# Kernel tuning notes

Hardware: AMD Instinct MI355X
Metric: run time of the kernel (lower is better)

Reference implementation:

```python
import jax, jax.numpy as jnp
import numpy as np

N_NODES = 100000
N_EDGES = 1600000
IN_CH = 64
HID = 64
N_GRAPHS = 64


def _sage_conv(x, src, dst, Wl, bl, Wr, n_nodes):
    # PyG SAGEConv (aggr='mean'): out = lin_l(mean_{j in N(i)} x_j) + lin_r(x_i)
    msg = x[src]                                            # [E, d] gather
    agg = jax.ops.segment_sum(msg, dst, num_segments=n_nodes)
    cnt = jax.ops.segment_sum(jnp.ones((src.shape[0],), x.dtype), dst,
                              num_segments=n_nodes)
    agg = agg / jnp.maximum(cnt, 1.0)[:, None]
    return agg @ Wl + bl + x @ Wr


def setup_inputs() -> dict:
    key = jax.random.key(0)
    ks = jax.random.split(key, 16)
    x = jax.random.normal(ks[0], (N_NODES, IN_CH), jnp.float32)
    edge_index = jax.random.randint(ks[1], (2, N_EDGES), 0, N_NODES, jnp.int64)
    batch = jnp.sort(jax.random.randint(ks[2], (N_NODES,), 0, N_GRAPHS, jnp.int64))

    def glorot(k, fan_in, fan_out):
        s = jnp.sqrt(2.0 / (fan_in + fan_out))
        return jax.random.normal(k, (fan_in, fan_out), jnp.float32) * s

    params = {
        'W1l': glorot(ks[3], IN_CH, HID), 'b1': jnp.zeros((HID,), jnp.float32),
        'W1r': glorot(ks[4], IN_CH, HID),
        'W2l': glorot(ks[5], HID, HID), 'b2': jnp.zeros((HID,), jnp.float32),
        'W2r': glorot(ks[6], HID, HID),
        'W3l': glorot(ks[7], HID, HID), 'b3': jnp.zeros((HID,), jnp.float32),
        'W3r': glorot(ks[8], HID, HID),
        'Wc1': glorot(ks[9], HID, HID // 2), 'bc1': jnp.zeros((HID // 2,), jnp.float32),
        'Wc2': glorot(ks[10], HID // 2, 2), 'bc2': jnp.zeros((2,), jnp.float32),
    }
    return {'x': x, 'edge_index': edge_index, 'batch': batch, **params}


def reference(x, edge_index, batch,
              W1l, b1, W1r, W2l, b2, W2r, W3l, b3, W3r,
              Wc1, bc1, Wc2, bc2):
    src, dst = edge_index[0], edge_index[1]
    n = x.shape[0]
    h = jax.nn.relu(_sage_conv(x, src, dst, W1l, b1, W1r, n))   # dropout = identity (eval)
    h = jax.nn.relu(_sage_conv(h, src, dst, W2l, b2, W2r, n))
    h = jax.nn.relu(_sage_conv(h, src, dst, W3l, b3, W3r, n))
    # global mean pool over graphs
    sums = jax.ops.segment_sum(h, batch, num_segments=N_GRAPHS)
    cnts = jax.ops.segment_sum(jnp.ones((n,), h.dtype), batch, num_segments=N_GRAPHS)
    g = sums / jnp.maximum(cnts, 1.0)[:, None]                  # [G, HID]
    # MLP head (dropout = identity at eval)
    return jax.nn.relu(g @ Wc1 + bc1) @ Wc2 + bc2               # [G, 2]
```

## Files before the change

kernel.cpp:

```cpp
#include <hip/hip_runtime.h>
#include <hip/hip_bf16.h>
#include <hip/hip_fp16.h>

typedef unsigned int u32;
typedef unsigned short u16;
typedef _Float16 f16x8 __attribute__((ext_vector_type(8)));
typedef float f32x4 __attribute__((ext_vector_type(4)));

#define NBLK1 512
#define MMBLK 256

__device__ __forceinline__ u16 f2h(float f) { return __half_as_ushort(__float2half(f)); }
__device__ __forceinline__ u32 packh2(float a, float b) {
    return (u32)f2h(a) | ((u32)f2h(b) << 16);
}
__device__ __forceinline__ __half2 sx(__half2 v, int m) {
    int iv = __shfl_xor(*(int*)&v, m, 64);
    return *(__half2*)&iv;
}

__device__ __forceinline__ int gidx(const void* p, long long i, int w64) {
    if (w64) return (int)((const long long*)p)[i];
    return ((const int*)p)[i];
}

__device__ __forceinline__ int detect_w64(const int* edge_words, int E, int tid, int* sh) {
    if (tid == 0) *sh = 0;
    __syncthreads();
    const long long totalWords = 2LL * E;
    const long long step = totalWords / 256;
    long long w = ((long long)tid * step) | 1;
    int nz = (w < totalWords) ? edge_words[w] : 0;
    if (nz) atomicOr(sh, 1);
    __syncthreads();
    return (*sh) ? 0 : 1;
}

__global__ void __launch_bounds__(256) fused_hist_mm1(
        const void* __restrict__ edge, int* __restrict__ flag, u32* __restrict__ ticket,
        u32* __restrict__ HG, int E, int n, int nb1,
        const float* __restrict__ X, const float* __restrict__ Wl,
        const float* __restrict__ Wr, const float* __restrict__ Bv,
        u16* __restrict__ Z, u16* __restrict__ R) {
    if (blockIdx.x < NBLK1) {
        __shared__ u32 h[256];
        __shared__ int shnz;
        const int tid = threadIdx.x;
        h[tid] = 0;
        const int w64 = detect_w64((const int*)edge, E, tid, &shnz);
        if (blockIdx.x == 0 && tid == 0) { flag[0] = w64; ticket[0] = 0; }
        __syncthreads();
        const int chunk = (E + NBLK1 - 1) / NBLK1;
        const int s = blockIdx.x * chunk;
        const int e = min(s + chunk, E);
        for (int i = s + tid; i < e; i += 256) {
            int d = gidx(edge, (long long)E + i, w64);
            if ((unsigned)d >= (unsigned)n) d = 0;
            atomicAdd(&h[d >> 9], 1);
        }
        __syncthreads();
        for (int b = tid; b < nb1; b += 256) HG[b * NBLK1 + blockIdx.x] = h[b];
        return;
    }
    const int lane = threadIdx.x & 63;
    const int quad = lane >> 4;
    const int m16 = lane & 15;
    f16x8 bl[2][4], br[2][4];
#pragma unroll
    for (int kh = 0; kh < 2; ++kh)
#pragma unroll
        for (int t = 0; t < 4; ++t)
#pragma unroll
            for (int j = 0; j < 8; ++j) {
                int k = kh * 32 + quad * 8 + j;
                int c = t * 16 + m16;
                bl[kh][t][j] = (_Float16)Wl[k * 64 + c];
                br[kh][t][j] = (_Float16)Wr[k * 64 + c];
            }
    float bias_t[4];
#pragma unroll
    for (int t = 0; t < 4; ++t) bias_t[t] = Bv[t * 16 + m16];

    const int ntiles = (n + 15) >> 4;
    const int nwaves = (gridDim.x - NBLK1) * 4;
    for (int tile = (blockIdx.x - NBLK1) * 4 + (threadIdx.x >> 6); tile < ntiles; tile += nwaves) {
        const int nodeBase = tile << 4;
        int nodeA = nodeBase + m16;
        if (nodeA >= n) nodeA = n - 1;
        f16x8 a[2];
#pragma unroll
        for (int kh = 0; kh < 2; ++kh) {
            const float4* p = (const float4*)(X + (size_t)nodeA * 64 + kh * 32 + quad * 8);
            float4 x0 = p[0], x1 = p[1];
            a[kh][0] = (_Float16)x0.x; a[kh][1] = (_Float16)x0.y;
            a[kh][2] = (_Float16)x0.z; a[kh][3] = (_Float16)x0.w;
            a[kh][4] = (_Float16)x1.x; a[kh][5] = (_Float16)x1.y;
            a[kh][6] = (_Float16)x1.z; a[kh][7] = (_Float16)x1.w;
        }
        f32x4 cl[4], cr[4];
#pragma unroll
        for (int t = 0; t < 4; ++t) {
            f32x4 c0 = {0.f, 0.f, 0.f, 0.f};
            c0 = __builtin_amdgcn_mfma_f32_16x16x32_f16(a[0], bl[0][t], c0, 0, 0, 0);
            c0 = __builtin_amdgcn_mfma_f32_16x16x32_f16(a[1], bl[1][t], c0, 0, 0, 0);
            cl[t] = c0;
            f32x4 c1 = {0.f, 0.f, 0.f, 0.f};
            c1 = __builtin_amdgcn_mfma_f32_16x16x32_f16(a[0], br[0][t], c1, 0, 0, 0);
            c1 = __builtin_amdgcn_mfma_f32_16x16x32_f16(a[1], br[1][t], c1, 0, 0, 0);
            cr[t] = c1;
        }
#pragma unroll
        for (int rg = 0; rg < 4; ++rg) {
            const int node = nodeBase + quad * 4 + rg;
            if (node < n) {
#pragma unroll
                for (int t = 0; t < 4; ++t) {
                    const int c = t * 16 + m16;
                    Z[(size_t)node * 64 + c] = f2h(cl[t][rg]);
                    R[(size_t)node * 64 + c] = f2h(cr[t][rg] + bias_t[t]);
                }
            }
        }
    }
}

__global__ void scanAB(u32* __restrict__ HG, u32* __restrict__ blockSums,
                       u32* __restrict__ SB, u32* __restrict__ ticket, int n) {
    __shared__ u32 ts[256];
    __shared__ int isLast;
    const int ITEMS = 8;
    const int tid = threadIdx.x;
    int base = blockIdx.x * 2048 + tid * ITEMS;
    u32 v[ITEMS];
    u32 sum = 0;
#pragma unroll
    for (int i = 0; i < ITEMS; ++i) {
        int idx = base + i;
        v[i] = (idx < n) ? HG[idx] : 0;
        sum += v[i];
    }
    ts[tid] = sum;
    __syncthreads();
    u32 incl = sum;
    for (int d = 1; d < 256; d <<= 1) {
        u32 y = 0;
        if (tid >= d) y = ts[tid - d];
        __syncthreads();
        incl += y;
        ts[tid] = incl;
        __syncthreads();
    }
    u32 run = incl - sum;
#pragma unroll
    for (int i = 0; i < ITEMS; ++i) {
        int idx = base + i;
        if (idx < n) HG[idx] = run;
        run += v[i];
    }
    if (tid == 255) {
        atomicExch(&blockSums[blockIdx.x], incl);
        __threadfence();
        u32 t = atomicAdd(&ticket[0], 1u);
        isLast = (t == gridDim.x - 1);
    }
    __syncthreads();
    if (!isLast) return;
    const int nb = gridDim.x;
    u32 bv = (tid < nb) ? atomicAdd(&blockSums[tid], 0u) : 0;
    ts[tid] = bv;
    __syncthreads();
    u32 bincl = bv;
    for (int d = 1; d < 256; d <<= 1) {
        u32 y = 0;
        if (tid >= d) y = ts[tid - d];
        __syncthreads();
        bincl += y;
        ts[tid] = bincl;
        __syncthreads();
    }
    if (tid < nb) SB[tid] = bincl - bv;
}

__global__ void __launch_bounds__(256) p1_scatter(const void* __restrict__ edge,
                                                  const int* __restrict__ flag,
                                                  const u32* __restrict__ HG,
                                                  const u32* __restrict__ SB,
                                                  u32* __restrict__ P, int E, int n, int nb1) {
    __shared__ u32 base[256];
    __shared__ u32 cur[256];
    const int tid = threadIdx.x;
    cur[tid] = 0;
    for (int b = tid; b < nb1; b += 256) {
        int i = b * NBLK1 + blockIdx.x;
        base[b] = HG[i] + SB[i >> 11];
    }
    __syncthreads();
    const int w64 = flag[0];
    const int chunk = (E + NBLK1 - 1) / NBLK1;
    const int s = blockIdx.x * chunk;
    const int e = min(s + chunk, E);
    for (int i = s + tid; i < e; i += 256) {
        int d = gidx(edge, (long long)E + i, w64);
        if ((unsigned)d >= (unsigned)n) d = 0;
        int sv = gidx(edge, i, w64);
        if ((unsigned)sv >= (unsigned)n) sv = 0;
        const int b1 = d >> 9;
        u32 r = atomicAdd(&cur[b1], 1);
        P[base[b1] + r] = (u32)sv | ((u32)(d & 511) << 17);
    }
}

__global__ void __launch_bounds__(256) p2_kernel(const u32* __restrict__ P,
                                                 const u32* __restrict__ HG,
                                                 const u32* __restrict__ SB,
                                                 u32* __restrict__ offs,
                                                 int* __restrict__ ss,
                                                 float* __restrict__ pool,
                                                 int E, int n, int nb1) {
    __shared__ u32 h2[512];
    __shared__ u32 ts[256];
    const int tid = threadIdx.x;
    const int b = blockIdx.x;
    if (b == 0)
        for (int i = tid; i < 4096; i += 256) pool[i] = 0.f;
    const int i0 = b * NBLK1;
    const int bs = (int)(HG[i0] + SB[i0 >> 11]);
    int be;
    if (b + 1 < nb1) {
        const int i1 = (b + 1) * NBLK1;
        be = (int)(HG[i1] + SB[i1 >> 11]);
    } else be = E;
    h2[tid] = 0;
    h2[tid + 256] = 0;
    __syncthreads();
    for (int i = bs + tid; i < be; i += 256) atomicAdd(&h2[(P[i] >> 17) & 511], 1);
    __syncthreads();
    u32 v0 = h2[2 * tid], v1 = h2[2 * tid + 1];
    u32 sum = v0 + v1;
    ts[tid] = sum;
    __syncthreads();
    u32 incl = sum;
    for (int d = 1; d < 256; d <<= 1) {
        u32 y = 0;
        if (tid >= d) y = ts[tid - d];
        __syncthreads();
        incl += y;
        ts[tid] = incl;
        __syncthreads();
    }
    u32 run = incl - sum;
    h2[2 * tid] = run;
    h2[2 * tid + 1] = run + v0;
    const int node0 = b * 512 + 2 * tid;
    if (node0 < n) offs[node0] = bs + run;
    if (node0 + 1 < n) offs[node0 + 1] = bs + run + v0;
    if (b == 0 && tid == 0) offs[n] = (u32)E;
    __syncthreads();
    for (int i = bs + tid; i < be; i += 256) {
        u32 p = P[i];
        u32 r = atomicAdd(&h2[(p >> 17) & 511], 1);
        ss[bs + r] = (int)(p & 0x1FFFFu);
    }
}

__global__ void __launch_bounds__(256) mm_mfma_kernel(const u16* __restrict__ X,
                                                      const float* __restrict__ Wl,
                                                      const float* __restrict__ Wr,
                                                      const float* __restrict__ Bv,
                                                      u16* __restrict__ Z,
                                                      u16* __restrict__ R, int n) {
    const int lane = threadIdx.x & 63;
    const int quad = lane >> 4;
    const int m16 = lane & 15;
    f16x8 bl[2][4], br[2][4];
#pragma unroll
    for (int kh = 0; kh < 2; ++kh)
#pragma unroll
        for (int t = 0; t < 4; ++t)
#pragma unroll
            for (int j = 0; j < 8; ++j) {
                int k = kh * 32 + quad * 8 + j;
                int c = t * 16 + m16;
                bl[kh][t][j] = (_Float16)Wl[k * 64 + c];
                br[kh][t][j] = (_Float16)Wr[k * 64 + c];
            }
    float bias_t[4];
#pragma unroll
    for (int t = 0; t < 4; ++t) bias_t[t] = Bv[t * 16 + m16];

    const int ntiles = (n + 15) >> 4;
    const int nwaves = gridDim.x * 4;
    for (int tile = blockIdx.x * 4 + (threadIdx.x >> 6); tile < ntiles; tile += nwaves) {
        const int nodeBase = tile << 4;
        int nodeA = nodeBase + m16;
        if (nodeA >= n) nodeA = n - 1;
        const _Float16* xp = (const _Float16*)X + (size_t)nodeA * 64;
        f16x8 a[2];
#pragma unroll
        for (int kh = 0; kh < 2; ++kh)
            a[kh] = *(const f16x8*)(xp + kh * 32 + quad * 8);
        f32x4 cl[4], cr[4];
#pragma unroll
        for (int t = 0; t < 4; ++t) {
            f32x4 c0 = {0.f, 0.f, 0.f, 0.f};
            c0 = __builtin_amdgcn_mfma_f32_16x16x32_f16(a[0], bl[0][t], c0, 0, 0, 0);
            c0 = __builtin_amdgcn_mfma_f32_16x16x32_f16(a[1], bl[1][t], c0, 0, 0, 0);
            cl[t] = c0;
            f32x4 c1 = {0.f, 0.f, 0.f, 0.f};
            c1 = __builtin_amdgcn_mfma_f32_16x16x32_f16(a[0], br[0][t], c1, 0, 0, 0);
            c1 = __builtin_amdgcn_mfma_f32_16x16x32_f16(a[1], br[1][t], c1, 0, 0, 0);
            cr[t] = c1;
        }
#pragma unroll
        for (int rg = 0; rg < 4; ++rg) {
            const int node = nodeBase + quad * 4 + rg;
            if (node < n) {
#pragma unroll
                for (int t = 0; t < 4; ++t) {
                    const int c = t * 16 + m16;
                    Z[(size_t)node * 64 + c] = f2h(cl[t][rg]);
                    R[(size_t)node * 64 + c] = f2h(cr[t][rg] + bias_t[t]);
                }
            }
        }
    }
}

__global__ void __launch_bounds__(256) agg_kernel(const u16* __restrict__ Zin,
                                                  const u16* __restrict__ Rin,
                                                  const u32* __restrict__ offs,
                                                  const int* __restrict__ ss,
                                                  u16* __restrict__ Hout, int n) {
    const int lane = threadIdx.x & 63;
    const int oct = lane >> 3;
    const int sub = lane & 7;
    const uint4* Z16 = (const uint4*)Zin;
    const int node = (blockIdx.x << 2) | (threadIdx.x >> 6);
    if (node >= n) return;
    const int off = (int)offs[node], end = (int)offs[node + 1];
    const int deg = end - off;
    const __half2 zero2 = __float2half2_rn(0.f);
    const __half2 one2 = __float2half2_rn(1.f);
    __half2 a0 = zero2, a1 = zero2, a2 = zero2, a3 = zero2;
    __half2 b0 = zero2, b1 = zero2, b2 = zero2, b3 = zero2;
    for (int base = off; base < end; base += 64) {
        const int cnt = min(64, end - base);
        const int idx = ss[base + (lane < cnt ? lane : cnt - 1)];
        int p = 0;
        for (; p + 16 <= cnt; p += 16) {
            int s0 = __shfl(idx, p + oct, 64);
            int s1 = __shfl(idx, p + 8 + oct, 64);
            uint4 u0 = Z16[(size_t)s0 * 8 + sub];
            uint4 u1 = Z16[(size_t)s1 * 8 + sub];
            a0 = __hadd2(a0, *(const __half2*)&u0.x);
            a1 = __hadd2(a1, *(const __half2*)&u0.y);
            a2 = __hadd2(a2, *(const __half2*)&u0.z);
            a3 = __hadd2(a3, *(const __half2*)&u0.w);
            b0 = __hadd2(b0, *(const __half2*)&u1.x);
            b1 = __hadd2(b1, *(const __half2*)&u1.y);
            b2 = __hadd2(b2, *(const __half2*)&u1.z);
            b3 = __hadd2(b3, *(const __half2*)&u1.w);
        }
        const int rem = cnt - p;
        if (rem) {
            int j = p + oct;
            int s0 = __shfl(idx, j < cnt ? j : cnt - 1, 64);
            uint4 u0 = Z16[(size_t)s0 * 8 + sub];
            __half2 m0 = (j < cnt) ? one2 : zero2;
            a0 = __hfma2(*(const __half2*)&u0.x, m0, a0);
            a1 = __hfma2(*(const __half2*)&u0.y, m0, a1);
            a2 = __hfma2(*(const __half2*)&u0.z, m0, a2);
            a3 = __hfma2(*(const __half2*)&u0.w, m0, a3);
            if (rem > 8) {
                int j1 = p + 8 + oct;
                int s1 = __shfl(idx, j1 < cnt ? j1 : cnt - 1, 64);
                uint4 u1 = Z16[(size_t)s1 * 8 + sub];
                __half2 m1 = (j1 < cnt) ? one2 : zero2;
                b0 = __hfma2(*(const __half2*)&u1.x, m1, b0);
                b1 = __hfma2(*(const __half2*)&u1.y, m1, b1);
                b2 = __hfma2(*(const __half2*)&u1.z, m1, b2);
                b3 = __hfma2(*(const __half2*)&u1.w, m1, b3);
            }
        }
    }
    a0 = __hadd2(a0, b0); a1 = __hadd2(a1, b1);
    a2 = __hadd2(a2, b2); a3 = __hadd2(a3, b3);
    a0 = __hadd2(a0, sx(a0, 8));  a1 = __hadd2(a1, sx(a1, 8));
    a2 = __hadd2(a2, sx(a2, 8));  a3 = __hadd2(a3, sx(a3, 8));
    a0 = __hadd2(a0, sx(a0, 16)); a1 = __hadd2(a1, sx(a1, 16));
    a2 = __hadd2(a2, sx(a2, 16)); a3 = __hadd2(a3, sx(a3, 16));
    a0 = __hadd2(a0, sx(a0, 32)); a1 = __hadd2(a1, sx(a1, 32));
    a2 = __hadd2(a2, sx(a2, 32)); a3 = __hadd2(a3, sx(a3, 32));
    if (oct == 0) {
        const uint4* R16 = (const uint4*)Rin;
        uint4 rr = R16[(size_t)node * 8 + sub];
        const float rd = deg > 0 ? 1.f / (float)deg : 0.f;
        float2 sA = __half22float2(a0), rA = __half22float2(*(const __half2*)&rr.x);
        float2 sB = __half22float2(a1), rB = __half22float2(*(const __half2*)&rr.y);
        float2 sC = __half22float2(a2), rC = __half22float2(*(const __half2*)&rr.z);
        float2 sD = __half22float2(a3), rD = __half22float2(*(const __half2*)&rr.w);
        uint4 outp;
        outp.x = packh2(fmaxf(fmaf(sA.x, rd, rA.x), 0.f), fmaxf(fmaf(sA.y, rd, rA.y), 0.f));
        outp.y = packh2(fmaxf(fmaf(sB.x, rd, rB.x), 0.f), fmaxf(fmaf(sB.y, rd, rB.y), 0.f));
        outp.z = packh2(fmaxf(fmaf(sC.x, rd, rC.x), 0.f), fmaxf(fmaf(sC.y, rd, rC.y), 0.f));
        outp.w = packh2(fmaxf(fmaf(sD.x, rd, rD.x), 0.f), fmaxf(fmaf(sD.y, rd, rD.y), 0.f));
        *(uint4*)(((u32*)Hout) + (size_t)node * 32 + 4 * sub) = outp;
    }
}

__global__ void pool_kernel(const u16* __restrict__ H, const void* __restrict__ batch,
                            const int* __restrict__ flag, float* __restrict__ pool, int n) {
    const int lane = threadIdx.x & 63;
    const int wave = threadIdx.x >> 6;
    int start = (blockIdx.x * 4 + wave) * 64;
    int end = min(start + 64, n);
    if (start >= end) return;
    const int w64 = flag[0];
    float acc = 0.f;
    int cur = gidx(batch, start, w64) & 63;
    for (int i = start; i < end; ++i) {
        int g = gidx(batch, i, w64) & 63;
        if (g != cur) {
            atomicAdd(&pool[cur * 64 + lane], acc);
            acc = 0.f;
            cur = g;
        }
        acc += __half2float(__ushort_as_half(H[i * 64 + lane]));
    }
    atomicAdd(&pool[cur * 64 + lane], acc);
}

__global__ void head_kernel(const float* __restrict__ pool, const void* __restrict__ batch,
                            const int* __restrict__ flag,
                            const float* __restrict__ Wc1, const float* __restrict__ bc1,
                            const float* __restrict__ Wc2, const float* __restrict__ bc2,
                            float* __restrict__ out, int n) {
    __shared__ float gm[64 * 64];
    __shared__ float am[64 * 32];
    __shared__ int cnts[64];
    const int tid = threadIdx.x;
    const int w64 = flag[0];
    if (tid < 64) {
        int lo = 0, hi = n;
        while (lo < hi) { int mid = (lo + hi) >> 1; if (gidx(batch, mid, w64) < tid) lo = mid + 1; else hi = mid; }
        int lo2 = 0, hi2 = n;
        int v2 = tid + 1;
        while (lo2 < hi2) { int mid = (lo2 + hi2) >> 1; if (gidx(batch, mid, w64) < v2) lo2 = mid + 1; else hi2 = mid; }
        cnts[tid] = lo2 - lo;
    }
    __syncthreads();
    for (int i = tid; i < 4096; i += 256) {
        int g = i >> 6;
        float c = (float)(cnts[g] > 0 ? cnts[g] : 1);
        gm[i] = pool[i] / c;
    }
    __syncthreads();
    for (int i = tid; i < 64 * 32; i += 256) {
        int g = i >> 5, j = i & 31;
        float acc = bc1[j];
        for (int k = 0; k < 64; ++k) acc += gm[g * 64 + k] * Wc1[k * 32 + j];
        am[i] = acc > 0.f ? acc : 0.f;
    }
    __syncthreads();
    if (tid < 128) {
        int g = tid >> 1, o = tid & 1;
        float acc = bc2[o];
        for (int j = 0; j < 32; ++j) acc += am[g * 32 + j] * Wc2[j * 2 + o];
        out[tid] = acc;
    }
}

extern "C" void kernel_launch(void* const* d_in, const int* in_sizes, int n_in,
                              void* d_out, int out_size, void* d_ws, size_t ws_size,
                              hipStream_t stream) {
    const float* x   = (const float*)d_in[0];
    const void* edge = d_in[1];
    const void* batch = d_in[2];
    const float* W1l = (const float*)d_in[3];
    const float* b1  = (const float*)d_in[4];
    const float* W1r = (const float*)d_in[5];
    const float* W2l = (const float*)d_in[6];
    const float* b2  = (const float*)d_in[7];
    const float* W2r = (const float*)d_in[8];
    const float* W3l = (const float*)d_in[9];
    const float* b3  = (const float*)d_in[10];
    const float* W3r = (const float*)d_in[11];
    const float* Wc1 = (const float*)d_in[12];
    const float* bc1 = (const float*)d_in[13];
    const float* Wc2 = (const float*)d_in[14];
    const float* bc2 = (const float*)d_in[15];

    const int n = in_sizes[0] / 64;
    const int E = in_sizes[1] / 2;
    const int nb1 = (n + 511) >> 9;
    const int NS = nb1 * NBLK1;

    char* w = (char*)d_ws;
    size_t o = 0;
    auto take = [&](size_t bytes) -> void* {
        void* p = w + o;
        o = (o + bytes + 511) & ~(size_t)511;
        return p;
    };
    int* flag      = (int*)take(sizeof(int));
    u32* ticket    = (u32*)take(2 * sizeof(u32));
    u32* offs      = (u32*)take((size_t)(n + 1) * sizeof(u32));
    u32* HG        = (u32*)take((size_t)(NS + 1) * sizeof(u32));
    u32* blockSums = (u32*)take(256 * sizeof(u32));
    u32* SB        = (u32*)take(256 * sizeof(u32));
    u32* P         = (u32*)take((size_t)E * sizeof(u32));
    int* ss        = (int*)take((size_t)E * sizeof(int));
    u16* Z         = (u16*)take((size_t)n * 64 * sizeof(u16));
    u16* R         = (u16*)take((size_t)n * 64 * sizeof(u16));
    u16* HA        = (u16*)take((size_t)n * 64 * sizeof(u16));
    u16* HB        = (u16*)take((size_t)n * 64 * sizeof(u16));
    float* pool    = (float*)take(64 * 64 * sizeof(float));

    fused_hist_mm1<<<NBLK1 + MMBLK, 256, 0, stream>>>(edge, flag, ticket, HG, E, n, nb1,
                                                      x, W1l, W1r, b1, Z, R);
    const int nbScan = (NS + 2047) / 2048;
    scanAB<<<nbScan, 256, 0, stream>>>(HG, blockSums, SB, ticket, NS);
    p1_scatter<<<NBLK1, 256, 0, stream>>>(edge, flag, HG, SB, P, E, n, nb1);
    p2_kernel<<<nb1, 256, 0, stream>>>(P, HG, SB, offs, ss, pool, E, n, nb1);

    const int nodeBlocks = (n + 3) / 4;
    agg_kernel<<<nodeBlocks, 256, 0, stream>>>(Z, R, offs, ss, HA, n);
    mm_mfma_kernel<<<MMBLK, 256, 0, stream>>>(HA, W2l, W2r, b2, Z, R, n);
    agg_kernel<<<nodeBlocks, 256, 0, stream>>>(Z, R, offs, ss, HB, n);
    mm_mfma_kernel<<<MMBLK, 256, 0, stream>>>(HB, W3l, W3r, b3, Z, R, n);
    agg_kernel<<<nodeBlocks, 256, 0, stream>>>(Z, R, offs, ss, HA, n);

    pool_kernel<<<(n + 255) / 256, 256, 0, stream>>>(HA, batch, flag, pool, n);
    head_kernel<<<1, 256, 0, stream>>>(pool, batch, flag, Wc1, bc1, Wc2, bc2,
                                       (float*)d_out, n);
}
```

Baseline: 331.7 us.

## Fuse mean aggregation, both GEMMs and pooling into per-layer SAGE kernel

Replaces the project-then-aggregate pipeline (mm kernel writing Z/R, then a separate agg kernel) with one sage_layer kernel per layer. Each wave gathers neighbor rows for 16 nodes, averages them in fp16, and runs the Wl and Wr MFMAs with bias and ReLU fused in. The last layer pools straight into the graph sums, so the separate pool kernel goes away. The first kernel now only converts x to fp16 alongside the histogram, and p2 moves to 512 threads with one node per thread. The cost is that the gather now uses one lane-quad per node instead of a full wave, which may lower memory-level parallelism, and it aggregates raw 64-wide features rather than pre-projected ones.

```diff
diff --git a/kernel.cpp b/kernel.cpp
--- a/kernel.cpp
+++ b/kernel.cpp
@@ -8,15 +8,11 @@
 typedef float f32x4 __attribute__((ext_vector_type(4)));
 
 #define NBLK1 512
-#define MMBLK 256
+#define CVTBLK 256
 
 __device__ __forceinline__ u16 f2h(float f) { return __half_as_ushort(__float2half(f)); }
 __device__ __forceinline__ u32 packh2(float a, float b) {
     return (u32)f2h(a) | ((u32)f2h(b) << 16);
-}
-__device__ __forceinline__ __half2 sx(__half2 v, int m) {
-    int iv = __shfl_xor(*(int*)&v, m, 64);
-    return *(__half2*)&iv;
 }
 
 __device__ __forceinline__ int gidx(const void* p, long long i, int w64) {
@@ -36,12 +32,10 @@
     return (*sh) ? 0 : 1;
 }
 
-__global__ void __launch_bounds__(256) fused_hist_mm1(
+__global__ void __launch_bounds__(256) fused_hist_cvt(
         const void* __restrict__ edge, int* __restrict__ flag, u32* __restrict__ ticket,
         u32* __restrict__ HG, int E, int n, int nb1,
-        const float* __restrict__ X, const float* __restrict__ Wl,
-        const float* __restrict__ Wr, const float* __restrict__ Bv,
-        u16* __restrict__ Z, u16* __restrict__ R) {
+        const float* __restrict__ X, u16* __restrict__ Xh) {
     if (blockIdx.x < NBLK1) {
         __shared__ u32 h[256];
         __shared__ int shnz;
@@ -62,65 +56,17 @@
         for (int b = tid; b < nb1; b += 256) HG[b * NBLK1 + blockIdx.x] = h[b];
         return;
     }
-    const int lane = threadIdx.x & 63;
-    const int quad = lane >> 4;
-    const int m16 = lane & 15;
-    f16x8 bl[2][4], br[2][4];
-#pragma unroll
-    for (int kh = 0; kh < 2; ++kh)
-#pragma unroll
-        for (int t = 0; t < 4; ++t)
-#pragma unroll
-            for (int j = 0; j < 8; ++j) {
-                int k = kh * 32 + quad * 8 + j;
-                int c = t * 16 + m16;
-                bl[kh][t][j] = (_Float16)Wl[k * 64 + c];
-                br[kh][t][j] = (_Float16)Wr[k * 64 + c];
-            }
-    float bias_t[4];
-#pragma unroll
-    for (int t = 0; t < 4; ++t) bias_t[t] = Bv[t * 16 + m16];
-
-    const int ntiles = (n + 15) >> 4;
-    const int nwaves = (gridDim.x - NBLK1) * 4;
-    for (int tile = (blockIdx.x - NBLK1) * 4 + (threadIdx.x >> 6); tile < ntiles; tile += nwaves) {
-        const int nodeBase = tile << 4;
-        int nodeA = nodeBase + m16;
-        if (nodeA >= n) nodeA = n - 1;
-        f16x8 a[2];
-#pragma unroll
-        for (int kh = 0; kh < 2; ++kh) {
-            const float4* p = (const float4*)(X + (size_t)nodeA * 64 + kh * 32 + quad * 8);
-            float4 x0 = p[0], x1 = p[1];
-            a[kh][0] = (_Float16)x0.x; a[kh][1] = (_Float16)x0.y;
-            a[kh][2] = (_Float16)x0.z; a[kh][3] = (_Float16)x0.w;
-            a[kh][4] = (_Float16)x1.x; a[kh][5] = (_Float16)x1.y;
-            a[kh][6] = (_Float16)x1.z; a[kh][7] = (_Float16)x1.w;
-        }
-        f32x4 cl[4], cr[4];
-#pragma unroll
-        for (int t = 0; t < 4; ++t) {
-            f32x4 c0 = {0.f, 0.f, 0.f, 0.f};
-            c0 = __builtin_amdgcn_mfma_f32_16x16x32_f16(a[0], bl[0][t], c0, 0, 0, 0);
-            c0 = __builtin_amdgcn_mfma_f32_16x16x32_f16(a[1], bl[1][t], c0, 0, 0, 0);
-            cl[t] = c0;
-            f32x4 c1 = {0.f, 0.f, 0.f, 0.f};
-            c1 = __builtin_amdgcn_mfma_f32_16x16x32_f16(a[0], br[0][t], c1, 0, 0, 0);
-            c1 = __builtin_amdgcn_mfma_f32_16x16x32_f16(a[1], br[1][t], c1, 0, 0, 0);
-            cr[t] = c1;
-        }
-#pragma unroll
-        for (int rg = 0; rg < 4; ++rg) {
-            const int node = nodeBase + quad * 4 + rg;
-            if (node < n) {
-#pragma unroll
-                for (int t = 0; t < 4; ++t) {
-                    const int c = t * 16 + m16;
-                    Z[(size_t)node * 64 + c] = f2h(cl[t][rg]);
-                    R[(size_t)node * 64 + c] = f2h(cr[t][rg] + bias_t[t]);
-                }
-            }
-        }
+    const long long total4 = (long long)n * 16;
+    const long long stride = (long long)CVTBLK * 256;
+    long long i = (long long)(blockIdx.x - NBLK1) * 256 + threadIdx.x;
+    const float4* X4 = (const float4*)X;
+    uint2* O = (uint2*)Xh;
+    for (; i < total4; i += stride) {
+        float4 v = X4[i];
+        uint2 o;
+        o.x = packh2(v.x, v.y);
+        o.y = packh2(v.z, v.w);
+        O[i] = o;
     }
 }
 
@@ -210,7 +156,7 @@
     }
 }
 
-__global__ void __launch_bounds__(256) p2_kernel(const u32* __restrict__ P,
+__global__ void __launch_bounds__(512) p2_kernel(const u32* __restrict__ P,
                                                  const u32* __restrict__ HG,
                                                  const u32* __restrict__ SB,
                                                  u32* __restrict__ offs,
@@ -218,11 +164,11 @@
                                                  float* __restrict__ pool,
                                                  int E, int n, int nb1) {
     __shared__ u32 h2[512];
-    __shared__ u32 ts[256];
+    __shared__ u32 ts[512];
     const int tid = threadIdx.x;
     const int b = blockIdx.x;
     if (b == 0)
-        for (int i = tid; i < 4096; i += 256) pool[i] = 0.f;
+        for (int i = tid; i < 4096; i += 512) pool[i] = 0.f;
     const int i0 = b * NBLK1;
     const int bs = (int)(HG[i0] + SB[i0 >> 11]);
     int be;
@@ -231,16 +177,14 @@
         be = (int)(HG[i1] + SB[i1 >> 11]);
     } else be = E;
     h2[tid] = 0;
-    h2[tid + 256] = 0;
-    __syncthreads();
-    for (int i = bs + tid; i < be; i += 256) atomicAdd(&h2[(P[i] >> 17) & 511], 1);
-    __syncthreads();
-    u32 v0 = h2[2 * tid], v1 = h2[2 * tid + 1];
-    u32 sum = v0 + v1;
-    ts[tid] = sum;
-    __syncthreads();
-    u32 incl = sum;
-    for (int d = 1; d < 256; d <<= 1) {
+    __syncthreads();
+    for (int i = bs + tid; i < be; i += 512) atomicAdd(&h2[(P[i] >> 17) & 511], 1);
+    __syncthreads();
+    u32 v = h2[tid];
+    ts[tid] = v;
+    __syncthreads();
+    u32 incl = v;
+    for (int d = 1; d < 512; d <<= 1) {
         u32 y = 0;
         if (tid >= d) y = ts[tid - d];
         __syncthreads();
@@ -248,27 +192,27 @@
         ts[tid] = incl;
         __syncthreads();
     }
-    u32 run = incl - sum;
-    h2[2 * tid] = run;
-    h2[2 * tid + 1] = run + v0;
-    const int node0 = b * 512 + 2 * tid;
+    u32 run = incl - v;
+    h2[tid] = run;
+    const int node0 = b * 512 + tid;
     if (node0 < n) offs[node0] = bs + run;
-    if (node0 + 1 < n) offs[node0 + 1] = bs + run + v0;
     if (b == 0 && tid == 0) offs[n] = (u32)E;
     __syncthreads();
-    for (int i = bs + tid; i < be; i += 256) {
+    for (int i = bs + tid; i < be; i += 512) {
         u32 p = P[i];
         u32 r = atomicAdd(&h2[(p >> 17) & 511], 1);
         ss[bs + r] = (int)(p & 0x1FFFFu);
     }
 }
 
-__global__ void __launch_bounds__(256) mm_mfma_kernel(const u16* __restrict__ X,
-                                                      const float* __restrict__ Wl,
-                                                      const float* __restrict__ Wr,
-                                                      const float* __restrict__ Bv,
-                                                      u16* __restrict__ Z,
-                                                      u16* __restrict__ R, int n) {
+__global__ void __launch_bounds__(256) sage_layer(
+        const u16* __restrict__ G, const u32* __restrict__ offs,
+        const int* __restrict__ ss,
+        const float* __restrict__ Wl, const float* __restrict__ Wr,
+        const float* __restrict__ Bv,
+        u16* __restrict__ Hout, float* __restrict__ pool,
+        const void* __restrict__ batch, const int* __restrict__ flag,
+        int n, int mode) {
     const int lane = threadIdx.x & 63;
     const int quad = lane >> 4;
     const int m16 = lane & 15;
@@ -287,147 +231,93 @@
     float bias_t[4];
 #pragma unroll
     for (int t = 0; t < 4; ++t) bias_t[t] = Bv[t * 16 + m16];
+    const int w64 = mode ? flag[0] : 0;
 
     const int ntiles = (n + 15) >> 4;
     const int nwaves = gridDim.x * 4;
     for (int tile = blockIdx.x * 4 + (threadIdx.x >> 6); tile < ntiles; tile += nwaves) {
         const int nodeBase = tile << 4;
-        int nodeA = nodeBase + m16;
-        if (nodeA >= n) nodeA = n - 1;
-        const _Float16* xp = (const _Float16*)X + (size_t)nodeA * 64;
-        f16x8 a[2];
-#pragma unroll
-        for (int kh = 0; kh < 2; ++kh)
-            a[kh] = *(const f16x8*)(xp + kh * 32 + quad * 8);
-        f32x4 cl[4], cr[4];
+        const int node_m = nodeBase + m16;
+        const int nodeA = node_m < n ? node_m : n - 1;
+        const u32 o0 = offs[nodeA];
+        const u32 o1 = offs[nodeA + 1];
+        const int deg = node_m < n ? (int)(o1 - o0) : 0;
+        f16x8 s0, s1;
+#pragma unroll
+        for (int j = 0; j < 8; ++j) { s0[j] = (_Float16)0; s1[j] = (_Float16)0; }
+        int e = 0;
+        for (; e + 2 <= deg; e += 2) {
+            const int sA = ss[o0 + e];
+            const int sB = ss[o0 + e + 1];
+            const f16x8* pa = (const f16x8*)(G + ((size_t)sA << 6)) + quad;
+            const f16x8* pb = (const f16x8*)(G + ((size_t)sB << 6)) + quad;
+            f16x8 a0 = pa[0], a1 = pa[4];
+            f16x8 b0 = pb[0], b1 = pb[4];
+            s0 += a0; s1 += a1;
+            s0 += b0; s1 += b1;
+        }
+        if (e < deg) {
+            const int sA = ss[o0 + e];
+            const f16x8* pa = (const f16x8*)(G + ((size_t)sA << 6)) + quad;
+            s0 += pa[0]; s1 += pa[4];
+        }
+        const float rdf = deg > 0 ? 1.f / (float)deg : 0.f;
+        const _Float16 hrd = (_Float16)rdf;
+#pragma unroll
+        for (int j = 0; j < 8; ++j) { s0[j] *= hrd; s1[j] *= hrd; }
+        const f16x8 as0 = *(const f16x8*)(G + (size_t)nodeA * 64 + quad * 8);
+        const f16x8 as1 = *(const f16x8*)(G + (size_t)nodeA * 64 + 32 + quad * 8);
+        f32x4 c[4];
 #pragma unroll
         for (int t = 0; t < 4; ++t) {
-            f32x4 c0 = {0.f, 0.f, 0.f, 0.f};
-            c0 = __builtin_amdgcn_mfma_f32_16x16x32_f16(a[0], bl[0][t], c0, 0, 0, 0);
-            c0 = __builtin_amdgcn_mfma_f32_16x16x32_f16(a[1], bl[1][t], c0, 0, 0, 0);
-            cl[t] = c0;
-            f32x4 c1 = {0.f, 0.f, 0.f, 0.f};
-            c1 = __builtin_amdgcn_mfma_f32_16x16x32_f16(a[0], br[0][t], c1, 0, 0, 0);
-            c1 = __builtin_amdgcn_mfma_f32_16x16x32_f16(a[1], br[1][t], c1, 0, 0, 0);
-            cr[t] = c1;
+            f32x4 acc = {bias_t[t], bias_t[t], bias_t[t], bias_t[t]};
+            acc = __builtin_amdgcn_mfma_f32_16x16x32_f16(s0, bl[0][t], acc, 0, 0, 0);
+            acc = __builtin_amdgcn_mfma_f32_16x16x32_f16(s1, bl[1][t], acc, 0, 0, 0);
+            acc = __builtin_amdgcn_mfma_f32_16x16x32_f16(as0, br[0][t], acc, 0, 0, 0);
+            acc = __builtin_amdgcn_mfma_f32_16x16x32_f16(as1, br[1][t], acc, 0, 0, 0);
+            c[t] = acc;
         }
-#pragma unroll
-        for (int rg = 0; rg < 4; ++rg) {
-            const int node = nodeBase + quad * 4 + rg;
-            if (node < n) {
+        if (mode == 0) {
+#pragma unroll
+            for (int rg = 0; rg < 4; ++rg) {
+                const int node = nodeBase + quad * 4 + rg;
+                if (node < n) {
+#pragma unroll
+                    for (int t = 0; t < 4; ++t)
+                        Hout[(size_t)node * 64 + t * 16 + m16] = f2h(fmaxf(c[t][rg], 0.f));
+                }
+            }
+        } else {
+            float v[4][4];
+#pragma unroll
+            for (int t = 0; t < 4; ++t)
+#pragma unroll
+                for (int rg = 0; rg < 4; ++rg) v[t][rg] = fmaxf(c[t][rg], 0.f);
+            const int lastN = nodeBase + 15 < n ? nodeBase + 15 : n - 1;
+            const int g0 = gidx(batch, nodeBase, w64) & 63;
+            const int g1 = gidx(batch, lastN, w64) & 63;
+            if (nodeBase + 15 < n && g0 == g1) {
 #pragma unroll
                 for (int t = 0; t < 4; ++t) {
-                    const int c = t * 16 + m16;
-                    Z[(size_t)node * 64 + c] = f2h(cl[t][rg]);
-                    R[(size_t)node * 64 + c] = f2h(cr[t][rg] + bias_t[t]);
+                    float cs = v[t][0] + v[t][1] + v[t][2] + v[t][3];
+                    cs += __shfl_xor(cs, 16, 64);
+                    cs += __shfl_xor(cs, 32, 64);
+                    if (quad == 0) atomicAdd(&pool[g0 * 64 + t * 16 + m16], cs);
+                }
+            } else {
+#pragma unroll
+                for (int rg = 0; rg < 4; ++rg) {
+                    const int node = nodeBase + quad * 4 + rg;
+                    if (node < n) {
+                        const int g = gidx(batch, node, w64) & 63;
+#pragma unroll
+                        for (int t = 0; t < 4; ++t)
+                            atomicAdd(&pool[g * 64 + t * 16 + m16], v[t][rg]);
+                    }
                 }
             }
         }
     }
-}
-
-__global__ void __launch_bounds__(256) agg_kernel(const u16* __restrict__ Zin,
-                                                  const u16* __restrict__ Rin,
-                                                  const u32* __restrict__ offs,
-                                                  const int* __restrict__ ss,
-                                                  u16* __restrict__ Hout, int n) {
-    const int lane = threadIdx.x & 63;
-    const int oct = lane >> 3;
-    const int sub = lane & 7;
-    const uint4* Z16 = (const uint4*)Zin;
-    const int node = (blockIdx.x << 2) | (threadIdx.x >> 6);
-    if (node >= n) return;
-    const int off = (int)offs[node], end = (int)offs[node + 1];
-    const int deg = end - off;
-    const __half2 zero2 = __float2half2_rn(0.f);
-    const __half2 one2 = __float2half2_rn(1.f);
-    __half2 a0 = zero2, a1 = zero2, a2 = zero2, a3 = zero2;
-    __half2 b0 = zero2, b1 = zero2, b2 = zero2, b3 = zero2;
-    for (int base = off; base < end; base += 64) {
-        const int cnt = min(64, end - base);
-        const int idx = ss[base + (lane < cnt ? lane : cnt - 1)];
-        int p = 0;
-        for (; p + 16 <= cnt; p += 16) {
-            int s0 = __shfl(idx, p + oct, 64);
-            int s1 = __shfl(idx, p + 8 + oct, 64);
-            uint4 u0 = Z16[(size_t)s0 * 8 + sub];
-            uint4 u1 = Z16[(size_t)s1 * 8 + sub];
-            a0 = __hadd2(a0, *(const __half2*)&u0.x);
-            a1 = __hadd2(a1, *(const __half2*)&u0.y);
-            a2 = __hadd2(a2, *(const __half2*)&u0.z);
-            a3 = __hadd2(a3, *(const __half2*)&u0.w);
-            b0 = __hadd2(b0, *(const __half2*)&u1.x);
-            b1 = __hadd2(b1, *(const __half2*)&u1.y);
-            b2 = __hadd2(b2, *(const __half2*)&u1.z);
-            b3 = __hadd2(b3, *(const __half2*)&u1.w);
-        }
-        const int rem = cnt - p;
-        if (rem) {
-            int j = p + oct;
-            int s0 = __shfl(idx, j < cnt ? j : cnt - 1, 64);
-            uint4 u0 = Z16[(size_t)s0 * 8 + sub];
-            __half2 m0 = (j < cnt) ? one2 : zero2;
-            a0 = __hfma2(*(const __half2*)&u0.x, m0, a0);
-            a1 = __hfma2(*(const __half2*)&u0.y, m0, a1);
-            a2 = __hfma2(*(const __half2*)&u0.z, m0, a2);
-            a3 = __hfma2(*(const __half2*)&u0.w, m0, a3);
-            if (rem > 8) {
-                int j1 = p + 8 + oct;
-                int s1 = __shfl(idx, j1 < cnt ? j1 : cnt - 1, 64);
-                uint4 u1 = Z16[(size_t)s1 * 8 + sub];
-                __half2 m1 = (j1 < cnt) ? one2 : zero2;
-                b0 = __hfma2(*(const __half2*)&u1.x, m1, b0);
-                b1 = __hfma2(*(const __half2*)&u1.y, m1, b1);
-                b2 = __hfma2(*(const __half2*)&u1.z, m1, b2);
-                b3 = __hfma2(*(const __half2*)&u1.w, m1, b3);
-            }
-        }
-    }
-    a0 = __hadd2(a0, b0); a1 = __hadd2(a1, b1);
-    a2 = __hadd2(a2, b2); a3 = __hadd2(a3, b3);
-    a0 = __hadd2(a0, sx(a0, 8));  a1 = __hadd2(a1, sx(a1, 8));
-    a2 = __hadd2(a2, sx(a2, 8));  a3 = __hadd2(a3, sx(a3, 8));
-    a0 = __hadd2(a0, sx(a0, 16)); a1 = __hadd2(a1, sx(a1, 16));
-    a2 = __hadd2(a2, sx(a2, 16)); a3 = __hadd2(a3, sx(a3, 16));
-    a0 = __hadd2(a0, sx(a0, 32)); a1 = __hadd2(a1, sx(a1, 32));
-    a2 = __hadd2(a2, sx(a2, 32)); a3 = __hadd2(a3, sx(a3, 32));
-    if (oct == 0) {
-        const uint4* R16 = (const uint4*)Rin;
-        uint4 rr = R16[(size_t)node * 8 + sub];
-        const float rd = deg > 0 ? 1.f / (float)deg : 0.f;
-        float2 sA = __half22float2(a0), rA = __half22float2(*(const __half2*)&rr.x);
-        float2 sB = __half22float2(a1), rB = __half22float2(*(const __half2*)&rr.y);
-        float2 sC = __half22float2(a2), rC = __half22float2(*(const __half2*)&rr.z);
-        float2 sD = __half22float2(a3), rD = __half22float2(*(const __half2*)&rr.w);
-        uint4 outp;
-        outp.x = packh2(fmaxf(fmaf(sA.x, rd, rA.x), 0.f), fmaxf(fmaf(sA.y, rd, rA.y), 0.f));
-        outp.y = packh2(fmaxf(fmaf(sB.x, rd, rB.x), 0.f), fmaxf(fmaf(sB.y, rd, rB.y), 0.f));
-        outp.z = packh2(fmaxf(fmaf(sC.x, rd, rC.x), 0.f), fmaxf(fmaf(sC.y, rd, rC.y), 0.f));
-        outp.w = packh2(fmaxf(fmaf(sD.x, rd, rD.x), 0.f), fmaxf(fmaf(sD.y, rd, rD.y), 0.f));
-        *(uint4*)(((u32*)Hout) + (size_t)node * 32 + 4 * sub) = outp;
-    }
-}
-
-__global__ void pool_kernel(const u16* __restrict__ H, const void* __restrict__ batch,
-                            const int* __restrict__ flag, float* __restrict__ pool, int n) {
-    const int lane = threadIdx.x & 63;
-    const int wave = threadIdx.x >> 6;
-    int start = (blockIdx.x * 4 + wave) * 64;
-    int end = min(start + 64, n);
-    if (start >= end) return;
-    const int w64 = flag[0];
-    float acc = 0.f;
-    int cur = gidx(batch, start, w64) & 63;
-    for (int i = start; i < end; ++i) {
-        int g = gidx(batch, i, w64) & 63;
-        if (g != cur) {
-            atomicAdd(&pool[cur * 64 + lane], acc);
-            acc = 0.f;
-            cur = g;
-        }
-        acc += __half2float(__ushort_as_half(H[i * 64 + lane]));
-    }
-    atomicAdd(&pool[cur * 64 + lane], acc);
 }
 
 __global__ void head_kernel(const float* __restrict__ pool, const void* __restrict__ batch,
@@ -510,27 +400,26 @@
     u32* SB        = (u32*)take(256 * sizeof(u32));
     u32* P         = (u32*)take((size_t)E * sizeof(u32));
     int* ss        = (int*)take((size_t)E * sizeof(int));
-    u16* Z         = (u16*)take((size_t)n * 64 * sizeof(u16));
-    u16* R         = (u16*)take((size_t)n * 64 * sizeof(u16));
+    u16* Xh        = (u16*)take((size_t)n * 64 * sizeof(u16));
     u16* HA        = (u16*)take((size_t)n * 64 * sizeof(u16));
     u16* HB        = (u16*)take((size_t)n * 64 * sizeof(u16));
     float* pool    = (float*)take(64 * 64 * sizeof(float));
 
-    fused_hist_mm1<<<NBLK1 + MMBLK, 256, 0, stream>>>(edge, flag, ticket, HG, E, n, nb1,
-                                                      x, W1l, W1r, b1, Z, R);
+    fused_hist_cvt<<<NBLK1 + CVTBLK, 256, 0, stream>>>(edge, flag, ticket, HG, E, n, nb1,
+                                                       x, Xh);
     const int nbScan = (NS + 2047) / 2048;
     scanAB<<<nbScan, 256, 0, stream>>>(HG, blockSums, SB, ticket, NS);
     p1_scatter<<<NBLK1, 256, 0, stream>>>(edge, flag, HG, SB, P, E, n, nb1);
-    p2_kernel<<<nb1, 256, 0, stream>>>(P, HG, SB, offs, ss, pool, E, n, nb1);
-
-    const int nodeBlocks = (n + 3) / 4;
-    agg_kernel<<<nodeBlocks, 256, 0, stream>>>(Z, R, offs, ss, HA, n);
-    mm_mfma_kernel<<<MMBLK, 256, 0, stream>>>(HA, W2l, W2r, b2, Z, R, n);
-    agg_kernel<<<nodeBlocks, 256, 0, stream>>>(Z, R, offs, ss, HB, n);
-    mm_mfma_kernel<<<MMBLK, 256, 0, stream>>>(HB, W3l, W3r, b3, Z, R, n);
-    agg_kernel<<<nodeBlocks, 256, 0, stream>>>(Z, R, offs, ss, HA, n);
-
-    pool_kernel<<<(n + 255) / 256, 256, 0, stream>>>(HA, batch, flag, pool, n);
+    p2_kernel<<<nb1, 512, 0, stream>>>(P, HG, SB, offs, ss, pool, E, n, nb1);
+
+    const int ntiles = (n + 15) >> 4;
+    const int SLBLK = (ntiles + 3) >> 2;
+    sage_layer<<<SLBLK, 256, 0, stream>>>(Xh, offs, ss, W1l, W1r, b1, HA, nullptr,
+                                          batch, flag, n, 0);
+    sage_layer<<<SLBLK, 256, 0, stream>>>(HA, offs, ss, W2l, W2r, b2, HB, nullptr,
+                                          batch, flag, n, 0);
+    sage_layer<<<SLBLK, 256, 0, stream>>>(HB, offs, ss, W3l, W3r, b3, nullptr, pool,
+                                          batch, flag, n, 1);
     head_kernel<<<1, 256, 0, stream>>>(pool, batch, flag, Wc1, bc1, Wc2, bc2,
                                        (float*)d_out, n);
 }
```

New measurement: 306.3 us. -7.6%, faster.
